# Performance work log

Measured on AMD Instinct MI355X. Metric: run time of the kernel, lower is better.

Reference implementation:

```python
import jax, jax.numpy as jnp
import numpy as np

K_NN = 16   # default k in prototype_filter
ITERS = 3   # default iters in Slot_Attention.__init__


def setup_inputs() -> dict:
    key = jax.random.key(0)
    ks = jax.random.split(key, 6)
    B, N, M, C, L = 8, 1024, 4096, 512, 2
    scale = 1.0 / np.sqrt(C)
    return {
        "slots": jax.random.normal(ks[0], (B, N, C), jnp.float32),
        "ref_pt_list": jax.random.normal(ks[1], (L, B, M, C), jnp.float32),
        "Wq": jax.random.normal(ks[2], (C, C), jnp.float32) * scale,
        "Wk": jax.random.normal(ks[3], (C, C), jnp.float32) * scale,
        "Wv": jax.random.normal(ks[4], (C, C), jnp.float32) * scale,
        "Wo": jax.random.normal(ks[5], (C, C), jnp.float32) * scale,
    }


def _prototype_filter(slots, ref):
    # slots: (B, N, C), ref: (B, M, C) -> gathered prototypes (B, N, K, C)
    # cosine-similarity KNN (torch knn(): L2-normalize, matmul, topk over refs)
    nt = slots / jnp.linalg.norm(slots, axis=2, keepdims=True)
    nr = ref / jnp.linalg.norm(ref, axis=2, keepdims=True)
    corr = jnp.einsum('bnc,bmc->bnm', nt, nr)          # (B, N, M)
    _, idx = jax.lax.top_k(corr, K_NN)                  # (B, N, K)
    b_idx = jnp.arange(ref.shape[0])[:, None, None]     # (B, 1, 1)
    return ref[b_idx, idx]                              # (B, N, K, C)


def _fat(slots, protos, Wq, Wk, Wv, Wo):
    # Feature_Aggregation_Transformer stand-in: per-slot cross-attention over
    # its K nearest prototypes, with residual. slots (B,N,C), protos (B,N,K,C).
    C = slots.shape[-1]
    q = slots @ Wq                                      # (B, N, C)
    k = protos @ Wk                                     # (B, N, K, C)
    v = protos @ Wv                                     # (B, N, K, C)
    logits = jnp.einsum('bnc,bnkc->bnk', q, k) / jnp.sqrt(jnp.asarray(C, slots.dtype))
    attn = jax.nn.softmax(logits, axis=-1)              # (B, N, K)
    out = jnp.einsum('bnk,bnkc->bnc', attn, v) @ Wo
    return slots + out


def reference(slots, ref_pt_list, Wq, Wk, Wv, Wo):
    # Original prototype_filter overwrites its result every list iteration,
    # so only the last ref in ref_pt_list contributes to the output.
    ref = ref_pt_list[-1]                               # (B, M, C)
    for _ in range(ITERS):
        protos = _prototype_filter(slots, ref)          # (B, N, K, C)
        slots = _fat(slots, protos, Wq, Wk, Wv, Wo)     # (B, N, C)
    return slots
```

## Files before the change

### kernel.cpp

```cpp
#include <hip/hip_runtime.h>
#include <hip/hip_bf16.h>

#define B_    8
#define N_    1024
#define M_    4096
#define C_    512
#define KNN_  16
#define ITERS_ 3

typedef short short8 __attribute__((ext_vector_type(8)));
typedef float float4v __attribute__((ext_vector_type(4)));

__device__ __forceinline__ void gl16(const __hip_bfloat16* g, short* l) {
    __builtin_amdgcn_global_load_lds(
        (const __attribute__((address_space(1))) unsigned int*)g,
        (__attribute__((address_space(3))) unsigned int*)l, 16, 0, 0);
}

__global__ void f32_to_f64_k(const float* __restrict__ in,
                             double* __restrict__ out, int n) {
    int i = blockIdx.x * blockDim.x + threadIdx.x;
    int stride = gridDim.x * blockDim.x;
    for (; i < n; i += stride) out[i] = (double)in[i];
}

__global__ void f64_to_f32_k(const double* __restrict__ in,
                             float* __restrict__ out, int n) {
    int i = blockIdx.x * blockDim.x + threadIdx.x;
    int stride = gridDim.x * blockDim.x;
    for (; i < n; i += stride) out[i] = (float)in[i];
}

__global__ void norm_split_ref_k(const float* __restrict__ ref,
                                 double* __restrict__ invn, double* __restrict__ rn,
                                 __hip_bfloat16* __restrict__ hi, __hip_bfloat16* __restrict__ lo) {
    const int row = blockIdx.x, lane = threadIdx.x;
    const float* p = ref + (size_t)row * C_;
    double s = 0.0;
    for (int i = lane; i < C_; i += 64) { double v = (double)p[i]; s += v * v; }
    for (int o = 32; o > 0; o >>= 1) s += __shfl_down(s, o);
    s = __shfl(s, 0);
    if (lane == 0) { invn[row] = 1.0 / sqrt(s); rn[row] = sqrt(s); }
    const double inv = 1.0 / sqrt(s);
    for (int i = lane; i < C_; i += 64) {
        float x = (float)((double)p[i] * inv);
        __hip_bfloat16 h = __float2bfloat16(x);
        hi[(size_t)row * C_ + i] = h;
        lo[(size_t)row * C_ + i] = __float2bfloat16(x - __bfloat162float(h));
    }
}

__global__ void norm_split_slots_k(const double* __restrict__ slots,
                                   double* __restrict__ invn,
                                   __hip_bfloat16* __restrict__ hi, __hip_bfloat16* __restrict__ lo) {
    const int row = blockIdx.x, lane = threadIdx.x;
    const double* p = slots + (size_t)row * C_;
    double s = 0.0;
    for (int i = lane; i < C_; i += 64) { double v = p[i]; s += v * v; }
    for (int o = 32; o > 0; o >>= 1) s += __shfl_down(s, o);
    s = __shfl(s, 0);
    if (lane == 0) invn[row] = 1.0 / sqrt(s);
    const double inv = 1.0 / sqrt(s);
    for (int i = lane; i < C_; i += 64) {
        float x = (float)(p[i] * inv);
        __hip_bfloat16 h = __float2bfloat16(x);
        hi[(size_t)row * C_ + i] = h;
        lo[(size_t)row * C_ + i] = __float2bfloat16(x - __bfloat162float(h));
    }
}

__global__ void split_w_k(const float* __restrict__ Wk, const float* __restrict__ Wv,
                          __hip_bfloat16* __restrict__ kh, __hip_bfloat16* __restrict__ kl,
                          __hip_bfloat16* __restrict__ vh, __hip_bfloat16* __restrict__ vl) {
    int i = blockIdx.x * blockDim.x + threadIdx.x;
    int stride = gridDim.x * blockDim.x;
    for (; i < C_ * C_; i += stride) {
        int k = i >> 9, c = i & (C_ - 1);
        int o = c * C_ + k;
        float x = Wk[i];
        __hip_bfloat16 h = __float2bfloat16(x);
        kh[o] = h; kl[o] = __float2bfloat16(x - __bfloat162float(h));
        x = Wv[i];
        h = __float2bfloat16(x);
        vh[o] = h; vl[o] = __float2bfloat16(x - __bfloat162float(h));
    }
}

__global__ __launch_bounds__(256) void mfma_nt_k(const __hip_bfloat16* __restrict__ Ahi,
                                                 const __hip_bfloat16* __restrict__ Alo,
                                                 size_t strideAz,
                                                 const __hip_bfloat16* __restrict__ Bhi,
                                                 const __hip_bfloat16* __restrict__ Blo,
                                                 size_t strideBz,
                                                 float* __restrict__ C, size_t strideCz,
                                                 int J,
                                                 const double* __restrict__ rowScale) {
    __shared__ short AhS[128 * 32];
    __shared__ short AlS[128 * 32];
    __shared__ short BhS[128 * 32];
    __shared__ short BlS[128 * 32];
    const int z = blockIdx.z;
    const __hip_bfloat16* Ah = Ahi + (size_t)z * strideAz;
    const __hip_bfloat16* Al = Alo + (size_t)z * strideAz;
    const __hip_bfloat16* Bh = Bhi + (size_t)z * strideBz;
    const __hip_bfloat16* Bl = Blo + (size_t)z * strideBz;
    float* Cz = C + (size_t)z * strideCz;

    const int t = threadIdx.x;
    const int lane = t & 63, wid = t >> 6;
    const int quad = lane >> 4, l15 = lane & 15;
    const int wy = wid >> 1, wx = wid & 1;
    const int row0 = blockIdx.y * 128;
    const int col0 = blockIdx.x * 128;

    const int srow = wid * 16 + (lane >> 2);
    const int scol = (lane & 3) * 8;
    const size_t aoff0 = (size_t)(row0 + srow) * C_ + scol;
    const size_t aoff1 = (size_t)(row0 + 64 + srow) * C_ + scol;
    const size_t boff0 = (size_t)(col0 + srow) * C_ + scol;
    const size_t boff1 = (size_t)(col0 + 64 + srow) * C_ + scol;
    const int lds0 = srow * 32 + scol;
    const int lds1 = (64 + srow) * 32 + scol;

    float4v acc[4][4];
#pragma unroll
    for (int i = 0; i < 4; ++i)
#pragma unroll
        for (int j = 0; j < 4; ++j) acc[i][j] = (float4v){0.f, 0.f, 0.f, 0.f};

    for (int k0 = 0; k0 < C_; k0 += 32) {
        __syncthreads();
        gl16(Ah + aoff0 + k0, &AhS[lds0]);
        gl16(Ah + aoff1 + k0, &AhS[lds1]);
        gl16(Al + aoff0 + k0, &AlS[lds0]);
        gl16(Al + aoff1 + k0, &AlS[lds1]);
        gl16(Bh + boff0 + k0, &BhS[lds0]);
        gl16(Bh + boff1 + k0, &BhS[lds1]);
        gl16(Bl + boff0 + k0, &BlS[lds0]);
        gl16(Bl + boff1 + k0, &BlS[lds1]);
        __syncthreads();

        short8 ah[4], al[4], bh[4], bl[4];
#pragma unroll
        for (int rt = 0; rt < 4; ++rt) {
            int r = (wy * 64 + rt * 16 + l15) * 32 + quad * 8;
            ah[rt] = *(const short8*)&AhS[r];
            al[rt] = *(const short8*)&AlS[r];
        }
#pragma unroll
        for (int ct = 0; ct < 4; ++ct) {
            int r = (wx * 64 + ct * 16 + l15) * 32 + quad * 8;
            bh[ct] = *(const short8*)&BhS[r];
            bl[ct] = *(const short8*)&BlS[r];
        }
#pragma unroll
        for (int rt = 0; rt < 4; ++rt)
#pragma unroll
            for (int ct = 0; ct < 4; ++ct) {
                acc[rt][ct] = __builtin_amdgcn_mfma_f32_16x16x32_bf16(ah[rt], bh[ct], acc[rt][ct], 0, 0, 0);
                acc[rt][ct] = __builtin_amdgcn_mfma_f32_16x16x32_bf16(ah[rt], bl[ct], acc[rt][ct], 0, 0, 0);
                acc[rt][ct] = __builtin_amdgcn_mfma_f32_16x16x32_bf16(al[rt], bh[ct], acc[rt][ct], 0, 0, 0);
            }
    }

#pragma unroll
    for (int rt = 0; rt < 4; ++rt) {
        int mbase = row0 + wy * 64 + rt * 16 + quad * 4;
#pragma unroll
        for (int ct = 0; ct < 4; ++ct) {
            int n = col0 + wx * 64 + ct * 16 + l15;
#pragma unroll
            for (int reg = 0; reg < 4; ++reg) {
                float v = acc[rt][ct][reg];
                if (rowScale) v *= (float)rowScale[mbase + reg];
                Cz[(size_t)(mbase + reg) * J + n] = v;
            }
        }
    }
}

__global__ __launch_bounds__(256, 6) void select_rerank_k(const float* __restrict__ corr,
                                                          const double* __restrict__ slots,
                                                          const float* __restrict__ ref,
                                                          const double* __restrict__ inv_ns,
                                                          const double* __restrict__ inv_nr,
                                                          int* __restrict__ idx) {
    __shared__ unsigned hist[4096];
    __shared__ unsigned chunk[256];
    __shared__ double srow[C_];
    __shared__ unsigned thrBin;
    __shared__ int cnt;

    int* candIdx = (int*)hist;
    double* candV = (double*)&hist[256];

    const int row = blockIdx.x, t = threadIdx.x;
    const int bat = row >> 10;
    const float* crow = corr + (size_t)row * M_;
    const float* refb = ref + (size_t)bat * M_ * C_;
    const double* invB = inv_nr + (size_t)bat * M_;

    for (int i = t; i < 4096; i += 256) hist[i] = 0;
    {
        double ia = inv_ns[row];
        for (int i = t; i < C_; i += 256) srow[i] = slots[(size_t)row * C_ + i] * ia;
    }
    if (t == 0) cnt = 0;
    __syncthreads();

    const float4* crow4 = (const float4*)crow;
    float4 cf[4];
#pragma unroll
    for (int j = 0; j < 4; ++j) cf[j] = crow4[t + 256 * j];
    unsigned uv[16];
#pragma unroll
    for (int j = 0; j < 4; ++j) {
#pragma unroll
        for (int e = 0; e < 4; ++e) {
            unsigned u = __float_as_uint(((const float*)&cf[j])[e]);
            u = (u & 0x80000000u) ? ~u : (u | 0x80000000u);
            uv[j * 4 + e] = u;
            atomicAdd(&hist[u >> 20], 1u);
        }
    }
    __syncthreads();

    {
        unsigned s = 0;
        for (int b = t * 16; b < t * 16 + 16; ++b) s += hist[b];
        chunk[t] = s;
    }
    __syncthreads();
    if (t < 64) {
        unsigned v0 = chunk[t * 4 + 0], v1 = chunk[t * 4 + 1];
        unsigned v2 = chunk[t * 4 + 2], v3 = chunk[t * 4 + 3];
        unsigned tot = v0 + v1 + v2 + v3;
        unsigned incl = tot;
#pragma unroll
        for (int off = 1; off < 64; off <<= 1) {
            unsigned o = __shfl_down(incl, off);
            if (t + off < 64) incl += o;
        }
        unsigned excl = incl - tot;
        chunk[t * 4 + 3] = excl;
        chunk[t * 4 + 2] = excl + v3;
        chunk[t * 4 + 1] = excl + v3 + v2;
        chunk[t * 4 + 0] = excl + v3 + v2 + v1;
    }
    __syncthreads();
    {
        unsigned prev = chunk[t];
        for (int b = t * 16 + 15; b >= t * 16; --b) {
            unsigned cur = prev + hist[b];
            if (cur >= 32u && prev < 32u) thrBin = (unsigned)b;
            prev = cur;
        }
    }
    __syncthreads();

    const unsigned T = thrBin;
#pragma unroll
    for (int j = 0; j < 4; ++j) {
#pragma unroll
        for (int e = 0; e < 4; ++e) {
            if ((uv[j * 4 + e] >> 20) >= T) {
                int p = atomicAdd(&cnt, 1);
                if (p < 256) candIdx[p] = 1024 * j + 4 * t + e;
            }
        }
    }
    __syncthreads();
    const int nc = cnt < 256 ? cnt : 256;

    {
        const int w = t >> 6, l = t & 63;
        double sreg[8];
#pragma unroll
        for (int k = 0; k < 8; ++k) sreg[k] = srow[l + 64 * k];
        for (int cj = w; cj < nc; cj += 16) {
            int cc[4]; bool has[4]; const float* rp[4]; double ib[4];
#pragma unroll
            for (int q = 0; q < 4; ++q) {
                cc[q] = cj + 4 * q;
                has[q] = cc[q] < nc;
                int col = has[q] ? candIdx[cc[q]] : candIdx[cj];
                rp[q] = refb + (size_t)col * C_;
                ib[q] = has[q] ? invB[col] : 0.0;
            }
            double s[4] = {0.0, 0.0, 0.0, 0.0};
#pragma unroll
            for (int k = 0; k < 8; ++k) {
#pragma unroll
                for (int q = 0; q < 4; ++q)
                    s[q] += sreg[k] * ((double)rp[q][l + 64 * k] * ib[q]);
            }
#pragma unroll
            for (int o = 32; o > 0; o >>= 1) {
#pragma unroll
                for (int q = 0; q < 4; ++q) s[q] += __shfl_down(s[q], o);
            }
            if (l == 0) {
#pragma unroll
                for (int q = 0; q < 4; ++q)
                    if (has[q]) candV[cc[q]] = s[q];
            }
        }
    }
    __syncthreads();

    if (t < 64) {
        double v[4]; int g[4];
#pragma unroll
        for (int r = 0; r < 4; ++r) {
            int p = t + 64 * r;
            bool ok = p < nc;
            v[r] = ok ? candV[p] : -1e300;
            g[r] = ok ? candIdx[p] : 0x7fffffff;
        }
        int* orow = idx + (size_t)row * KNN_;
        for (int r = 0; r < KNN_; ++r) {
            double bv = v[0]; int bg = g[0];
#pragma unroll
            for (int q = 1; q < 4; ++q)
                if (v[q] > bv || (v[q] == bv && g[q] < bg)) { bv = v[q]; bg = g[q]; }
#pragma unroll
            for (int off = 32; off > 0; off >>= 1) {
                double ov = __shfl_xor(bv, off);
                int og = __shfl_xor(bg, off);
                if (ov > bv || (ov == bv && og < bg)) { bv = ov; bg = og; }
            }
            if (t == 0) orow[r] = bg;
#pragma unroll
            for (int q = 0; q < 4; ++q)
                if (g[q] == bg) v[q] = -1e300;
        }
    }
}

template <bool RES>
__global__ __launch_bounds__(256) void gemm_f64_k(const double* __restrict__ A,
                                                  const float* __restrict__ W,
                                                  const double* __restrict__ res,
                                                  double* __restrict__ out) {
    __shared__ double As[16][130];
    __shared__ double Bs[16][66];
    const int tx = threadIdx.x, ty = threadIdx.y;
    const int t = ty * 16 + tx;
    const int lk = t & 15, lr = t >> 4;
    const int wc = t & 63, wk = t >> 6;
    const int row0 = blockIdx.y * 128, col0 = blockIdx.x * 64;
    double acc[8][4] = {};
    for (int k0 = 0; k0 < C_; k0 += 16) {
#pragma unroll
        for (int p = 0; p < 8; ++p) {
            int r = lr + 16 * p;
            As[lk][r] = A[(size_t)(row0 + r) * C_ + k0 + lk];
        }
#pragma unroll
        for (int p = 0; p < 4; ++p)
            Bs[wk + 4 * p][wc] = (double)W[(size_t)(k0 + wk + 4 * p) * C_ + col0 + wc];
        __syncthreads();
#pragma unroll
        for (int kk = 0; kk < 16; ++kk) {
            double a[8], b[4];
#pragma unroll
            for (int i = 0; i < 8; ++i) a[i] = As[kk][ty * 8 + i];
#pragma unroll
            for (int j = 0; j < 4; ++j) b[j] = Bs[kk][tx * 4 + j];
#pragma unroll
            for (int i = 0; i < 8; ++i)
#pragma unroll
                for (int j = 0; j < 4; ++j) acc[i][j] += a[i] * b[j];
        }
        __syncthreads();
    }
#pragma unroll
    for (int i = 0; i < 8; ++i) {
        size_t r = row0 + ty * 8 + i;
#pragma unroll
        for (int j = 0; j < 4; ++j) {
            size_t o = r * C_ + col0 + tx * 4 + j;
            double v = acc[i][j];
            if (RES) v += res[o];
            out[o] = v;
        }
    }
}

__global__ __launch_bounds__(256) void attn_k(double* qo,
                                              const float* __restrict__ Kb,
                                              const float* __restrict__ Vb,
                                              const int* __restrict__ idx) {
    const int row = blockIdx.x;
    const int bat = row >> 10;
    const int t = threadIdx.x;
    const int lane = t & 63, w = t >> 6;
    __shared__ int sidx[KNN_];
    __shared__ double wred[4][KNN_];
    __shared__ double sw[KNN_];
    if (t < KNN_) sidx[t] = idx[(size_t)row * KNN_ + t];
    __syncthreads();
    double q0 = qo[(size_t)row * C_ + t];
    double q1 = qo[(size_t)row * C_ + t + 256];
    double p[KNN_];
#pragma unroll
    for (int j = 0; j < KNN_; ++j) {
        const float* kr = Kb + ((size_t)bat * M_ + sidx[j]) * C_;
        p[j] = q0 * (double)kr[t] + q1 * (double)kr[t + 256];
    }
#pragma unroll
    for (int j = 0; j < KNN_; ++j) {
        double s = p[j];
#pragma unroll
        for (int o = 32; o > 0; o >>= 1) s += __shfl_down(s, o);
        if (lane == 0) wred[w][j] = s;
    }
    __syncthreads();
    if (t < KNN_) {
        const double scale = 1.0 / sqrt((double)C_);
        double l = (wred[0][t] + wred[1][t] + wred[2][t] + wred[3][t]) * scale;
        double mx = l;
#pragma unroll
        for (int o = 8; o > 0; o >>= 1) {
            double om = __shfl_xor(mx, o, 16);
            mx = om > mx ? om : mx;
        }
        double e = exp(l - mx);
        double ssum = e;
#pragma unroll
        for (int o = 8; o > 0; o >>= 1) ssum += __shfl_xor(ssum, o, 16);
        sw[t] = e * (1.0 / ssum);
    }
    __syncthreads();
    double o0 = 0.0, o1 = 0.0;
#pragma unroll
    for (int j = 0; j < KNN_; ++j) {
        const float* vr = Vb + ((size_t)bat * M_ + sidx[j]) * C_;
        double wgt = sw[j];
        o0 += wgt * (double)vr[t];
        o1 += wgt * (double)vr[t + 256];
    }
    qo[(size_t)row * C_ + t] = o0;
    qo[(size_t)row * C_ + t + 256] = o1;
}

extern "C" void kernel_launch(void* const* d_in, const int* in_sizes, int n_in,
                              void* d_out, int out_size, void* d_ws, size_t ws_size,
                              hipStream_t stream) {
    const float* slots_in = (const float*)d_in[0];
    const float* reflist  = (const float*)d_in[1];
    const float* Wq = (const float*)d_in[2];
    const float* Wk = (const float*)d_in[3];
    const float* Wv = (const float*)d_in[4];
    const float* Wo = (const float*)d_in[5];
    const float* ref = reflist + ((size_t)in_sizes[1] - (size_t)B_ * M_ * C_);
    float* out = (float*)d_out;

    const size_t NR = (size_t)B_ * N_;
    const size_t MR = (size_t)B_ * M_;

    char* w = (char*)d_ws;
    double* slots_d = (double*)w;             w += NR * C_ * 8;
    float*  corr    = (float*)w;              w += NR * M_ * 4;
    float*  Kb      = (float*)w;              w += MR * C_ * 4;
    float*  Vb      = (float*)w;              w += MR * C_ * 4;
    __hip_bfloat16* Bhi = (__hip_bfloat16*)w; w += MR * C_ * 2;
    __hip_bfloat16* Blo = (__hip_bfloat16*)w; w += MR * C_ * 2;
    __hip_bfloat16* Ahi = (__hip_bfloat16*)w; w += NR * C_ * 2;
    __hip_bfloat16* Alo = (__hip_bfloat16*)w; w += NR * C_ * 2;
    __hip_bfloat16* Wkh = (__hip_bfloat16*)w; w += (size_t)C_ * C_ * 2;
    __hip_bfloat16* Wkl = (__hip_bfloat16*)w; w += (size_t)C_ * C_ * 2;
    __hip_bfloat16* Wvh = (__hip_bfloat16*)w; w += (size_t)C_ * C_ * 2;
    __hip_bfloat16* Wvl = (__hip_bfloat16*)w; w += (size_t)C_ * C_ * 2;
    double* inv_ns  = (double*)w;             w += NR * 8;
    double* inv_nr  = (double*)w;             w += MR * 8;
    double* rn      = (double*)w;             w += MR * 8;
    int*    idxb    = (int*)w;                w += NR * KNN_ * 4;
    double* qbuf    = (double*)corr;

    f32_to_f64_k<<<4096, 256, 0, stream>>>(slots_in, slots_d, (int)(NR * C_));
    norm_split_ref_k<<<(int)MR, 64, 0, stream>>>(ref, inv_nr, rn, Bhi, Blo);
    split_w_k<<<512, 256, 0, stream>>>(Wk, Wv, Wkh, Wkl, Wvh, Wvl);
    mfma_nt_k<<<dim3(C_ / 128, MR / 128, 1), 256, 0, stream>>>(
        Bhi, Blo, 0, Wkh, Wkl, 0, Kb, 0, C_, rn);
    mfma_nt_k<<<dim3(C_ / 128, MR / 128, 1), 256, 0, stream>>>(
        Bhi, Blo, 0, Wvh, Wvl, 0, Vb, 0, C_, rn);

    for (int it = 0; it < ITERS_; ++it) {
        norm_split_slots_k<<<(int)NR, 64, 0, stream>>>(slots_d, inv_ns, Ahi, Alo);
        mfma_nt_k<<<dim3(M_ / 128, N_ / 128, B_), 256, 0, stream>>>(
            Ahi, Alo, (size_t)N_ * C_, Bhi, Blo, (size_t)M_ * C_,
            corr, (size_t)N_ * M_, M_, nullptr);
        select_rerank_k<<<(int)NR, 256, 0, stream>>>(corr, slots_d, ref, inv_ns, inv_nr, idxb);
        gemm_f64_k<false><<<dim3(C_ / 64, NR / 128), dim3(16, 16), 0, stream>>>(
            slots_d, Wq, (const double*)nullptr, qbuf);
        attn_k<<<(int)NR, 256, 0, stream>>>(qbuf, Kb, Vb, idxb);
        gemm_f64_k<true><<<dim3(C_ / 64, NR / 128), dim3(16, 16), 0, stream>>>(
            qbuf, Wo, slots_d, slots_d);
    }

    f64_to_f32_k<<<4096, 256, 0, stream>>>(slots_d, out, (int)(NR * C_));
}
```

Baseline: 2.186 ms.

## Split select/rerank kernel and widen candidate threshold to 64 with cap 512

Splits the fused histogram-select and fp64 rerank kernel into two kernels that pass candidate indices through a global buffer. It also raises the histogram threshold from 32 to 64 candidates and the cap from 256 to 512. The larger pool makes the exact top-16 more robust to bf16-split approximation error. The cost is roughly twice the fp64 rerank work on gathered ref rows, plus an extra launch and a global round trip. Each kernel has lower register and LDS pressure, which may raise occupancy.

New measurement: 2.723 ms. 24.6% more time.

```diff
diff --git a/kernel.cpp b/kernel.cpp
--- a/kernel.cpp
+++ b/kernel.cpp
@@ -7,6 +7,7 @@
 #define C_    512
 #define KNN_  16
 #define ITERS_ 3
+#define CAND_CAP 512
 
 typedef short short8 __attribute__((ext_vector_type(8)));
 typedef float float4v __attribute__((ext_vector_type(4)));
@@ -179,36 +180,22 @@
     }
 }
 
-__global__ __launch_bounds__(256, 6) void select_rerank_k(const float* __restrict__ corr,
-                                                          const double* __restrict__ slots,
-                                                          const float* __restrict__ ref,
-                                                          const double* __restrict__ inv_ns,
-                                                          const double* __restrict__ inv_nr,
-                                                          int* __restrict__ idx) {
+__global__ __launch_bounds__(256) void select_hist_k(const float* __restrict__ corr,
+                                                     int* __restrict__ candIdx,
+                                                     int* __restrict__ candCnt) {
     __shared__ unsigned hist[4096];
     __shared__ unsigned chunk[256];
-    __shared__ double srow[C_];
     __shared__ unsigned thrBin;
     __shared__ int cnt;
 
-    int* candIdx = (int*)hist;
-    double* candV = (double*)&hist[256];
-
     const int row = blockIdx.x, t = threadIdx.x;
-    const int bat = row >> 10;
-    const float* crow = corr + (size_t)row * M_;
-    const float* refb = ref + (size_t)bat * M_ * C_;
-    const double* invB = inv_nr + (size_t)bat * M_;
+    const float4* crow4 = (const float4*)(corr + (size_t)row * M_);
+    int* crow_cand = candIdx + (size_t)row * CAND_CAP;
 
     for (int i = t; i < 4096; i += 256) hist[i] = 0;
-    {
-        double ia = inv_ns[row];
-        for (int i = t; i < C_; i += 256) srow[i] = slots[(size_t)row * C_ + i] * ia;
-    }
     if (t == 0) cnt = 0;
     __syncthreads();
 
-    const float4* crow4 = (const float4*)crow;
     float4 cf[4];
 #pragma unroll
     for (int j = 0; j < 4; ++j) cf[j] = crow4[t + 256 * j];
@@ -252,7 +239,7 @@
         unsigned prev = chunk[t];
         for (int b = t * 16 + 15; b >= t * 16; --b) {
             unsigned cur = prev + hist[b];
-            if (cur >= 32u && prev < 32u) thrBin = (unsigned)b;
+            if (cur >= 64u && prev < 64u) thrBin = (unsigned)b;
             prev = cur;
         }
     }
@@ -265,12 +252,38 @@
         for (int e = 0; e < 4; ++e) {
             if ((uv[j * 4 + e] >> 20) >= T) {
                 int p = atomicAdd(&cnt, 1);
-                if (p < 256) candIdx[p] = 1024 * j + 4 * t + e;
-            }
-        }
-    }
-    __syncthreads();
-    const int nc = cnt < 256 ? cnt : 256;
+                if (p < CAND_CAP) crow_cand[p] = 1024 * j + 4 * t + e;
+            }
+        }
+    }
+    __syncthreads();
+    if (t == 0) candCnt[row] = cnt < CAND_CAP ? cnt : CAND_CAP;
+}
+
+__global__ __launch_bounds__(256) void rerank_k(const double* __restrict__ slots,
+                                                const float* __restrict__ ref,
+                                                const double* __restrict__ inv_ns,
+                                                const double* __restrict__ inv_nr,
+                                                const int* __restrict__ candIdx,
+                                                const int* __restrict__ candCnt,
+                                                int* __restrict__ idx) {
+    __shared__ double srow[C_];
+    __shared__ int cIdx[CAND_CAP];
+    __shared__ double cV[CAND_CAP];
+
+    const int row = blockIdx.x, t = threadIdx.x;
+    const int bat = row >> 10;
+    const float* refb = ref + (size_t)bat * M_ * C_;
+    const double* invB = inv_nr + (size_t)bat * M_;
+    const int nc = candCnt[row];
+    const int* crow_cand = candIdx + (size_t)row * CAND_CAP;
+
+    {
+        double ia = inv_ns[row];
+        for (int i = t; i < C_; i += 256) srow[i] = slots[(size_t)row * C_ + i] * ia;
+    }
+    for (int i = t; i < nc; i += 256) cIdx[i] = crow_cand[i];
+    __syncthreads();
 
     {
         const int w = t >> 6, l = t & 63;
@@ -283,7 +296,7 @@
             for (int q = 0; q < 4; ++q) {
                 cc[q] = cj + 4 * q;
                 has[q] = cc[q] < nc;
-                int col = has[q] ? candIdx[cc[q]] : candIdx[cj];
+                int col = has[q] ? cIdx[cc[q]] : cIdx[cj];
                 rp[q] = refb + (size_t)col * C_;
                 ib[q] = has[q] ? invB[col] : 0.0;
             }
@@ -302,26 +315,26 @@
             if (l == 0) {
 #pragma unroll
                 for (int q = 0; q < 4; ++q)
-                    if (has[q]) candV[cc[q]] = s[q];
+                    if (has[q]) cV[cc[q]] = s[q];
             }
         }
     }
     __syncthreads();
 
     if (t < 64) {
-        double v[4]; int g[4];
-#pragma unroll
-        for (int r = 0; r < 4; ++r) {
+        double v[8]; int g[8];
+#pragma unroll
+        for (int r = 0; r < 8; ++r) {
             int p = t + 64 * r;
             bool ok = p < nc;
-            v[r] = ok ? candV[p] : -1e300;
-            g[r] = ok ? candIdx[p] : 0x7fffffff;
+            v[r] = ok ? cV[p] : -1e300;
+            g[r] = ok ? cIdx[p] : 0x7fffffff;
         }
         int* orow = idx + (size_t)row * KNN_;
         for (int r = 0; r < KNN_; ++r) {
             double bv = v[0]; int bg = g[0];
 #pragma unroll
-            for (int q = 1; q < 4; ++q)
+            for (int q = 1; q < 8; ++q)
                 if (v[q] > bv || (v[q] == bv && g[q] < bg)) { bv = v[q]; bg = g[q]; }
 #pragma unroll
             for (int off = 32; off > 0; off >>= 1) {
@@ -331,7 +344,7 @@
             }
             if (t == 0) orow[r] = bg;
 #pragma unroll
-            for (int q = 0; q < 4; ++q)
+            for (int q = 0; q < 8; ++q)
                 if (g[q] == bg) v[q] = -1e300;
         }
     }
@@ -476,6 +489,8 @@
     double* inv_nr  = (double*)w;             w += MR * 8;
     double* rn      = (double*)w;             w += MR * 8;
     int*    idxb    = (int*)w;                w += NR * KNN_ * 4;
+    int*    candI   = (int*)w;                w += NR * CAND_CAP * 4;
+    int*    candC   = (int*)w;                w += NR * 4;
     double* qbuf    = (double*)corr;
 
     f32_to_f64_k<<<4096, 256, 0, stream>>>(slots_in, slots_d, (int)(NR * C_));
@@ -491,7 +506,8 @@
         mfma_nt_k<<<dim3(M_ / 128, N_ / 128, B_), 256, 0, stream>>>(
             Ahi, Alo, (size_t)N_ * C_, Bhi, Blo, (size_t)M_ * C_,
             corr, (size_t)N_ * M_, M_, nullptr);
-        select_rerank_k<<<(int)NR, 256, 0, stream>>>(corr, slots_d, ref, inv_ns, inv_nr, idxb);
+        select_hist_k<<<(int)NR, 256, 0, stream>>>(corr, candI, candC);
+        rerank_k<<<(int)NR, 256, 0, stream>>>(slots_d, ref, inv_ns, inv_nr, candI, candC, idxb);
         gemm_f64_k<false><<<dim3(C_ / 64, NR / 128), dim3(16, 16), 0, stream>>>(
             slots_d, Wq, (const double*)nullptr, qbuf);
         attn_k<<<(int)NR, 256, 0, stream>>>(qbuf, Kb, Vb, idxb);
```
